# Kernel tuning notes

Hardware: AMD Instinct MI355X
Metric: run time of the kernel (lower is better)

## Reference

```python
import jax, jax.numpy as jnp
import numpy as np

NUM_HEADS = 4

def _pos_encoding(seq_len, d, dtype):
    # standard sinusoidal positional encoding [seq_len, d]
    pos = jnp.arange(seq_len, dtype=jnp.float32)[:, None]
    i = jnp.arange(0, d, 2, dtype=jnp.float32)
    div = jnp.exp(-jnp.log(10000.0) * i / d)
    ang = pos * div
    pe = jnp.zeros((seq_len, d), jnp.float32)
    pe = pe.at[:, 0::2].set(jnp.sin(ang)).at[:, 1::2].set(jnp.cos(ang))
    return pe.astype(dtype)

def _layer_norm(x, g, b, eps=1e-5):
    m = jnp.mean(x, axis=-1, keepdims=True)
    v = jnp.mean(jnp.square(x - m), axis=-1, keepdims=True)
    return (x - m) / jnp.sqrt(v + eps) * g + b

def setup_inputs() -> dict:
    key = jax.random.key(0)
    ks = jax.random.split(key, 10)
    B, S, H, W, N = 8, 512, 768, 8, 4096
    s = 0.02
    token_reps = jax.random.normal(ks[0], (B, S, H), jnp.float32)
    starts = jax.random.randint(ks[1], (B, N), 0, S - W)
    widths = jax.random.randint(ks[2], (B, N), 1, W + 1)
    span_ids = jnp.stack([starts, starts + widths], axis=-1)  # end > start, end <= S
    span_masks = jax.random.randint(ks[3], (B, N), 0, 2)
    return dict(
        token_reps=token_reps,
        dummy_query=jax.random.normal(ks[4], (H,), jnp.float32) * s,
        in_proj_w=jax.random.normal(ks[5], (3 * H, H), jnp.float32) * s,
        in_proj_b=jnp.zeros((3 * H,), jnp.float32),
        out_w=jax.random.normal(ks[6], (H, H), jnp.float32) * s,
        out_b=jnp.zeros((H,), jnp.float32),
        ln_g=jnp.ones((H,), jnp.float32),
        ln_b=jnp.zeros((H,), jnp.float32),
        ffn_w1=jax.random.normal(ks[7], (H, 4 * H), jnp.float32) * s,
        ffn_b1=jnp.zeros((4 * H,), jnp.float32),
        ffn_w2=jax.random.normal(ks[8], (4 * H, H), jnp.float32) * s,
        ffn_b2=jnp.zeros((H,), jnp.float32),
        span_ids=span_ids,
        span_masks=span_masks,
    )

def reference(token_reps, dummy_query, in_proj_w, in_proj_b, out_w, out_b,
              ln_g, ln_b, ffn_w1, ffn_b1, ffn_w2, ffn_b2, span_ids, span_masks):
    B, S, H = token_reps.shape
    N = span_ids.shape[1]
    NH = NUM_HEADS
    DH = H // NH
    # sequence positional encoding (dropout is identity in eval mode)
    x = token_reps + _pos_encoding(S, H, token_reps.dtype)[None]
    Wq, Wk, Wv = jnp.split(in_proj_w, 3, axis=0)
    bq, bk, bv = jnp.split(in_proj_b, 3)
    # single shared dummy query -> per-head query [NH, DH]
    q = (dummy_query @ Wq.T + bq).reshape(NH, DH)
    k = (x @ Wk.T + bk).reshape(B, S, NH, DH)
    v = (x @ Wv.T + bv).reshape(B, S, NH, DH)
    # scores are identical across spans since the query is shared: [B, NH, S]
    scores = jnp.einsum('hd,bshd->bhs', q, k) / jnp.sqrt(jnp.asarray(DH, x.dtype))
    pos = jnp.arange(S)
    # per-span key validity: start <= pos < end, and span not masked out  [B, N, S]
    valid = (pos[None, None, :] >= span_ids[..., 0:1]) & \
            (pos[None, None, :] < span_ids[..., 1:2]) & \
            (span_masks[..., None] != 0)
    logits = jnp.where(valid[:, :, None, :], scores[:, None, :, :], -1e9)  # [B,N,NH,S]
    w = jax.nn.softmax(logits, axis=-1)
    attn = jnp.einsum('bnhs,bshd->bnhd', w, v).reshape(B, N, H)
    attn = attn @ out_w.T + out_b
    h1 = _layer_norm(attn + dummy_query, ln_g, ln_b)
    ffn = jax.nn.relu(h1 @ ffn_w1 + ffn_b1) @ ffn_w2 + ffn_b2
    out = _layer_norm(ffn + h1, ln_g, ln_b)
    # masked spans produce exact zeros, matching the original loop
    return out * (span_masks[..., None] != 0).astype(out.dtype)
```

## Files before the change

kernel.cpp:

```cpp
#include <hip/hip_runtime.h>
#include <hip/hip_bf16.h>

#define Bb 8
#define Ss 512
#define Hh 768
#define NHh 4
#define Nn 4096
#define ROWS (Bb * Nn)
#define SCB 128

typedef _Float16 f16x8 __attribute__((ext_vector_type(8)));
typedef _Float16 f16x4 __attribute__((ext_vector_type(4)));
typedef _Float16 f16x2 __attribute__((ext_vector_type(2)));
typedef float f32x4 __attribute__((ext_vector_type(4)));

#define DEVINL __device__ __forceinline__

DEVINL void gld_lds16(const void* g, void* l) {
  __builtin_amdgcn_global_load_lds(
      (const __attribute__((address_space(1))) void*)g,
      (__attribute__((address_space(3))) void*)l, 16, 0, 0);
}

template <int V>
DEVINL void wait_vmcnt() {
  if constexpr (V == 0) asm volatile("s_waitcnt vmcnt(0)" ::: "memory");
  else if constexpr (V == 3) asm volatile("s_waitcnt vmcnt(3)" ::: "memory");
  else if constexpr (V == 4) asm volatile("s_waitcnt vmcnt(4)" ::: "memory");
  else if constexpr (V == 6) asm volatile("s_waitcnt vmcnt(6)" ::: "memory");
  else if constexpr (V == 8) asm volatile("s_waitcnt vmcnt(8)" ::: "memory");
}

DEVINL float block_sum256(float v, float* red) {
#pragma unroll
  for (int o = 32; o; o >>= 1) v += __shfl_xor(v, o, 64);
  const int wid = threadIdx.x >> 6, lane = threadIdx.x & 63;
  if (lane == 0) red[wid] = v;
  __syncthreads();
  float r = red[0] + red[1] + red[2] + red[3];
  __syncthreads();
  return r;
}

__global__ __launch_bounds__(256) void x_kernel(const float* __restrict__ tok,
                                                _Float16* __restrict__ x) {
  int idx = blockIdx.x * 256 + threadIdx.x;
  int t = idx % 384;
  int bs = idx / 384;
  int s = bs & (Ss - 1);
  float div = expf(-(float)t * 0.02398526138535465f);
  float ang = (float)s * div;
  float sv = sinf(ang), cv = cosf(ang);
  const float2 tv = ((const float2*)tok)[(size_t)bs * 384 + t];
  f16x2 o;
  o[0] = (_Float16)(tv.x + sv);
  o[1] = (_Float16)(tv.y + cv);
  *(f16x2*)&x[(size_t)bs * Hh + 2 * t] = o;
}

__global__ __launch_bounds__(256) void q_kernel(const float* __restrict__ dq,
                                                const float* __restrict__ ipw,
                                                const float* __restrict__ ipb,
                                                float* __restrict__ qout) {
  __shared__ float red[4];
  int o = blockIdx.x;
  const float* wr = ipw + (size_t)o * Hh;
  float s = 0.f;
#pragma unroll
  for (int e = 0; e < 3; e++) {
    int j = threadIdx.x + 256 * e;
    s += dq[j] * wr[j];
  }
  s = block_sum256(s, red);
  if (threadIdx.x == 0) qout[o] = s + ipb[o];
}

__global__ __launch_bounds__(256) void c_kernel(const float* __restrict__ q,
                                                const float* __restrict__ ipw,
                                                const float* __restrict__ ipb,
                                                float* __restrict__ cout,
                                                float* __restrict__ sbias) {
  __shared__ float red[4];
  int bid = blockIdx.x;
  int t = threadIdx.x;
  if (bid < 3072) {
    int h = bid / Hh;
    int j = bid - h * Hh;
    float s = 0.f;
    if (t < 192) s = q[h * 192 + t] * ipw[(size_t)(Hh + h * 192 + t) * Hh + j];
    s = block_sum256(s, red);
    if (t == 0) cout[bid] = s;
  } else {
    int h = bid - 3072;
    float s = 0.f;
    if (t < 192) s = q[h * 192 + t] * ipb[Hh + h * 192 + t];
    s = block_sum256(s, red);
    if (t == 0) sbias[h] = s;
  }
}

__global__ __launch_bounds__(256) void score_kernel(
    const _Float16* __restrict__ x, const float* __restrict__ c,
    const float* __restrict__ sbias, float* __restrict__ scores) {
  int bs = blockIdx.x;
  int wid = threadIdx.x >> 6, lane = threadIdx.x & 63;
  const _Float16* xr = x + (size_t)bs * Hh;
  const float* ch = c + wid * Hh;
  float s = 0.f;
#pragma unroll
  for (int e = 0; e < 12; e++) {
    int j = e * 64 + lane;
    s += (float)xr[j] * ch[j];
  }
#pragma unroll
  for (int o = 32; o; o >>= 1) s += __shfl_xor(s, o, 64);
  if (lane == 0) {
    int b = bs >> 9, pos = bs & (Ss - 1);
    scores[((size_t)(b * NHh + wid)) * Ss + pos] =
        (s + sbias[wid]) * 0.07216878364870322f;
  }
}

__global__ __launch_bounds__(256) void cvt_kernel(const float* __restrict__ in,
                                                  _Float16* __restrict__ out) {
  int i = blockIdx.x * 256 + threadIdx.x;
  float4 f = ((const float4*)in)[i];
  f16x4 o;
  o[0] = (_Float16)f.x;
  o[1] = (_Float16)f.y;
  o[2] = (_Float16)f.z;
  o[3] = (_Float16)f.w;
  ((f16x4*)out)[i] = o;
}

__global__ __launch_bounds__(256) void trcvt_kernel(const float* __restrict__ in,
                                                    _Float16* __restrict__ out,
                                                    int R, int C) {
  __shared__ float tile[32][33];
  int c0 = blockIdx.x * 32, r0 = blockIdx.y * 32;
  int tx = threadIdx.x & 31, ty0 = threadIdx.x >> 5;
#pragma unroll
  for (int ty = ty0; ty < 32; ty += 8)
    tile[ty][tx] = in[(size_t)(r0 + ty) * C + c0 + tx];
  __syncthreads();
#pragma unroll
  for (int ty = ty0; ty < 32; ty += 8)
    out[(size_t)(c0 + ty) * R + r0 + tx] = (_Float16)tile[tx][ty];
}

__global__ __launch_bounds__(256) void scan1_kernel(const int* __restrict__ mask,
                                                    int* __restrict__ bsum) {
  int r = blockIdx.x * 256 + threadIdx.x;
  unsigned long long b = __ballot(mask[r] != 0);
  __shared__ int wsum[4];
  int lane = threadIdx.x & 63, wid = threadIdx.x >> 6;
  if (lane == 0) wsum[wid] = __popcll(b);
  __syncthreads();
  if (threadIdx.x == 0)
    bsum[blockIdx.x] = wsum[0] + wsum[1] + wsum[2] + wsum[3];
}
__global__ __launch_bounds__(64) void scan2_kernel(const int* __restrict__ bsum,
                                                   int* __restrict__ boff,
                                                   int* __restrict__ cnt) {
  if (threadIdx.x == 0) {
    int acc = 0;
    for (int i = 0; i < SCB; i++) {
      boff[i] = acc;
      acc += bsum[i];
    }
    *cnt = acc;
  }
}
__global__ __launch_bounds__(256) void cidx_kernel(const int* __restrict__ mask,
                                                   const int* __restrict__ boff,
                                                   int* __restrict__ cidx) {
  int r = blockIdx.x * 256 + threadIdx.x;
  int m = mask[r] != 0;
  unsigned long long b = __ballot(m);
  __shared__ int wsum[4];
  int lane = threadIdx.x & 63, wid = threadIdx.x >> 6;
  if (lane == 0) wsum[wid] = __popcll(b);
  __syncthreads();
  int pre = 0;
#pragma unroll
  for (int i = 0; i < 3; i++)
    if (i < wid) pre += wsum[i];
  pre += __popcll(b & ((1ULL << lane) - 1));
  if (m) cidx[r] = boff[blockIdx.x] + pre;
}

template <int RELU, int BN>
__global__ __launch_bounds__(256, 2) void gemm_nt(
    const _Float16* __restrict__ A, const _Float16* __restrict__ W,
    const float* __restrict__ bias, _Float16* __restrict__ C, int N, int K,
    int nn, const int* __restrict__ mcount) {
  const int bid = (int)blockIdx.x;
  const int mi = (bid >> 3) / nn;
  const int nt_ = (bid >> 3) - mi * nn;
  const long m0 = (long)(mi * 8 + (bid & 7)) * 128;
  const long n0 = (long)nt_ * BN;
  if (mcount && m0 >= (long)*mcount) return;
  __shared__ __align__(16) _Float16 As[3][128 * 32];
  __shared__ __align__(16) _Float16 Bs[3][BN * 32];
  const int tid = threadIdx.x;
  const int wid = tid >> 6;
  const int lane = tid & 63;
  constexpr int LPS = (BN == 128) ? 4 : 3;

  const int c0 = wid * 64 + lane;
  const int c1 = c0 + 256;
  const int sw0 = ((c0 & 3) ^ ((c0 >> 3) & 3)) * 8;
  const int sw1 = ((c1 & 3) ^ ((c1 >> 3) & 3)) * 8;
  const _Float16* gA0 = A + (m0 + (c0 >> 2)) * K + sw0;
  const _Float16* gA1 = A + (m0 + (c1 >> 2)) * K + sw1;
  const _Float16* gB0 = W + (n0 + (c0 >> 2)) * K + sw0;
  const _Float16* gB1 = W + (n0 + (c1 >> 2)) * K + sw1;

  const int wr = (wid >> 1) * 64;
  const int wc = (wid & 1) * (BN / 2);
  constexpr int NF = BN / 32;
  const int fr = lane & 15;
  const int fkb = lane >> 4;

  f32x4 acc[4][NF];
#pragma unroll
  for (int mi2 = 0; mi2 < 4; mi2++)
#pragma unroll
    for (int ni = 0; ni < NF; ni++) acc[mi2][ni] = (f32x4){0.f, 0.f, 0.f, 0.f};

#define STAGE(buf, k0)                                                  \
  do {                                                                  \
    gld_lds16(gA0 + (k0), &As[buf][wid * 512]);                         \
    gld_lds16(gA1 + (k0), &As[buf][2048 + wid * 512]);                  \
    gld_lds16(gB0 + (k0), &Bs[buf][wid * 512]);                         \
    if constexpr (BN == 128) gld_lds16(gB1 + (k0), &Bs[buf][2048 + wid * 512]); \
  } while (0)

#define COMPUTE(buf)                                                          \
  do {                                                                        \
    f16x8 af[4], bf[NF];                                                      \
    _Pragma("unroll") for (int i = 0; i < 4; i++) {                           \
      int r_ = wr + i * 16 + fr;                                              \
      af[i] = *(const f16x8*)&As[buf][r_ * 32 + ((fkb ^ ((r_ >> 1) & 3)) * 8)]; \
    }                                                                         \
    _Pragma("unroll") for (int i = 0; i < NF; i++) {                          \
      int r_ = wc + i * 16 + fr;                                              \
      bf[i] = *(const f16x8*)&Bs[buf][r_ * 32 + ((fkb ^ ((r_ >> 1) & 3)) * 8)]; \
    }                                                                         \
    __builtin_amdgcn_s_setprio(1);                                            \
    _Pragma("unroll") for (int mi2 = 0; mi2 < 4; mi2++)                       \
        _Pragma("unroll") for (int ni = 0; ni < NF; ni++)                     \
            acc[mi2][ni] = __builtin_amdgcn_mfma_f32_16x16x32_f16(            \
                af[mi2], bf[ni], acc[mi2][ni], 0, 0, 0);                      \
    __builtin_amdgcn_s_setprio(0);                                            \
  } while (0)

#define ITER_RESTAGE(b, knext)              \
  do {                                      \
    wait_vmcnt<2 * LPS>();                  \
    __builtin_amdgcn_s_barrier();           \
    COMPUTE(b);                             \
    __builtin_amdgcn_s_barrier();           \
    STAGE(b, (knext));                      \
  } while (0)

  const int nt = K >> 5;
  STAGE(0, 0);
  STAGE(1, 32);
  STAGE(2, 64);
  int t = 0;
  for (; t <= nt - 6; t += 3) {
    ITER_RESTAGE(0, (t + 3) * 32);
    ITER_RESTAGE(1, (t + 4) * 32);
    ITER_RESTAGE(2, (t + 5) * 32);
  }
  wait_vmcnt<2 * LPS>();
  __builtin_amdgcn_s_barrier();
  COMPUTE(0);
  wait_vmcnt<LPS>();
  __builtin_amdgcn_s_barrier();
  COMPUTE(1);
  wait_vmcnt<0>();
  __builtin_amdgcn_s_barrier();
  COMPUTE(2);
#undef STAGE
#undef COMPUTE
#undef ITER_RESTAGE

  const int crow = (lane >> 4) * 4;
  const int ccol = lane & 15;
  float bv[NF];
#pragma unroll
  for (int ni = 0; ni < NF; ni++)
    bv[ni] = bias ? bias[n0 + wc + ni * 16 + ccol] : 0.f;
#pragma unroll
  for (int mi2 = 0; mi2 < 4; mi2++)
#pragma unroll
    for (int ni = 0; ni < NF; ni++)
#pragma unroll
      for (int i = 0; i < 4; i++) {
        float v = acc[mi2][ni][i] + bv[ni];
        if (RELU) v = fmaxf(v, 0.f);
        C[(m0 + wr + mi2 * 16 + crow + i) * (long)N + (n0 + wc + ni * 16 + ccol)] =
            (_Float16)v;
      }
}

template <int RELU>
__global__ __launch_bounds__(512, 4) void gemm8_nt(
    const _Float16* __restrict__ A, const _Float16* __restrict__ W,
    const float* __restrict__ bias, _Float16* __restrict__ C, int N, int K,
    int nn, const int* __restrict__ mcount) {
  const int bid = (int)blockIdx.x;
  const int mi = (bid >> 3) / nn;
  const int nt_ = (bid >> 3) - mi * nn;
  const long m0 = (long)(mi * 8 + (bid & 7)) * 256;
  const long n0 = (long)nt_ * 128;
  if (mcount && m0 >= (long)*mcount) return;
  __shared__ __align__(16) _Float16 As[3][256 * 32];
  __shared__ __align__(16) _Float16 Bs[3][128 * 32];
  const int tid = threadIdx.x;
  const int w = tid >> 6;
  const int lane = tid & 63;
  constexpr int LPS = 3;

  const int rA0 = w * 16 + (lane >> 2);
  const int rA1 = rA0 + 128;
  const int cb = lane & 3;
  const int swA0 = (cb ^ ((rA0 >> 1) & 3)) * 8;
  const int swA1 = (cb ^ ((rA1 >> 1) & 3)) * 8;
  const _Float16* gA0 = A + (m0 + rA0) * K + swA0;
  const _Float16* gA1 = A + (m0 + rA1) * K + swA1;
  const _Float16* gB0 = W + (n0 + rA0) * K + swA0;

  const int wr = (w >> 1) * 64;
  const int wc = (w & 1) * 64;
  const int fr = lane & 15;
  const int fkb = lane >> 4;

  f32x4 acc[4][4];
#pragma unroll
  for (int mi2 = 0; mi2 < 4; mi2++)
#pragma unroll
    for (int ni = 0; ni < 4; ni++) acc[mi2][ni] = (f32x4){0.f, 0.f, 0.f, 0.f};

#define STAGE(buf, k0)                                   \
  do {                                                   \
    gld_lds16(gA0 + (k0), &As[buf][w * 512]);            \
    gld_lds16(gA1 + (k0), &As[buf][(w + 8) * 512]);      \
    gld_lds16(gB0 + (k0), &Bs[buf][w * 512]);            \
  } while (0)

#define COMPUTE(buf)                                                          \
  do {                                                                        \
    f16x8 af[4], bf[4];                                                       \
    _Pragma("unroll") for (int i = 0; i < 4; i++) {                           \
      int r_ = wr + i * 16 + fr;                                              \
      af[i] = *(const f16x8*)&As[buf][r_ * 32 + ((fkb ^ ((r_ >> 1) & 3)) * 8)]; \
    }                                                                         \
    _Pragma("unroll") for (int i = 0; i < 4; i++) {                           \
      int r_ = wc + i * 16 + fr;                                              \
      bf[i] = *(const f16x8*)&Bs[buf][r_ * 32 + ((fkb ^ ((r_ >> 1) & 3)) * 8)]; \
    }                                                                         \
    __builtin_amdgcn_s_setprio(1);                                            \
    _Pragma("unroll") for (int mi2 = 0; mi2 < 4; mi2++)                       \
        _Pragma("unroll") for (int ni = 0; ni < 4; ni++)                      \
            acc[mi2][ni] = __builtin_amdgcn_mfma_f32_16x16x32_f16(            \
                af[mi2], bf[ni], acc[mi2][ni], 0, 0, 0);                      \
    __builtin_amdgcn_s_setprio(0);                                            \
  } while (0)

#define ITER_RESTAGE(b, knext)              \
  do {                                      \
    wait_vmcnt<2 * LPS>();                  \
    __builtin_amdgcn_s_barrier();           \
    COMPUTE(b);                             \
    __builtin_amdgcn_s_barrier();           \
    STAGE(b, (knext));                      \
  } while (0)

  const int nt = K >> 5;
  STAGE(0, 0);
  STAGE(1, 32);
  STAGE(2, 64);
  int t = 0;
  for (; t <= nt - 6; t += 3) {
    ITER_RESTAGE(0, (t + 3) * 32);
    ITER_RESTAGE(1, (t + 4) * 32);
    ITER_RESTAGE(2, (t + 5) * 32);
  }
  wait_vmcnt<2 * LPS>();
  __builtin_amdgcn_s_barrier();
  COMPUTE(0);
  wait_vmcnt<LPS>();
  __builtin_amdgcn_s_barrier();
  COMPUTE(1);
  wait_vmcnt<0>();
  __builtin_amdgcn_s_barrier();
  COMPUTE(2);
#undef STAGE
#undef COMPUTE
#undef ITER_RESTAGE

  const int crow = (lane >> 4) * 4;
  const int ccol = lane & 15;
  float bv[4];
#pragma unroll
  for (int ni = 0; ni < 4; ni++)
    bv[ni] = bias ? bias[n0 + wc + ni * 16 + ccol] : 0.f;
#pragma unroll
  for (int mi2 = 0; mi2 < 4; mi2++)
#pragma unroll
    for (int ni = 0; ni < 4; ni++)
#pragma unroll
      for (int i = 0; i < 4; i++) {
        float v = acc[mi2][ni][i] + bv[ni];
        if (RELU) v = fmaxf(v, 0.f);
        C[(m0 + wr + mi2 * 16 + crow + i) * (long)N + (n0 + wc + ni * 16 + ccol)] =
            (_Float16)v;
      }
}

template <int RELU>
__global__ __launch_bounds__(512, 2) void gemm16_nt(
    const _Float16* __restrict__ A, const _Float16* __restrict__ W,
    const float* __restrict__ bias, _Float16* __restrict__ C, int N, int K,
    int nn, const int* __restrict__ mcount) {
  const int bid = (int)blockIdx.x;
  const int mi = (bid >> 3) / nn;
  const int nt_ = (bid >> 3) - mi * nn;
  const long m0 = (long)(mi * 8 + (bid & 7)) * 256;
  const long n0 = (long)nt_ * 256;
  if (mcount && m0 >= (long)*mcount) return;
  __shared__ __align__(16) _Float16 As[3][256 * 32];
  __shared__ __align__(16) _Float16 Bs[3][256 * 32];
  const int tid = threadIdx.x;
  const int w = tid >> 6;
  const int lane = tid & 63;
  constexpr int LPS = 4;

  const int r0c = w * 16 + (lane >> 2);
  const int r1c = r0c + 128;
  const int cb = lane & 3;
  const int sw0 = (cb ^ ((r0c >> 1) & 3)) * 8;
  const int sw1 = (cb ^ ((r1c >> 1) & 3)) * 8;
  const _Float16* gA0 = A + (m0 + r0c) * K + sw0;
  const _Float16* gA1 = A + (m0 + r1c) * K + sw1;
  const _Float16* gB0 = W + (n0 + r0c) * K + sw0;
  const _Float16* gB1 = W + (n0 + r1c) * K + sw1;

  const int wr = (w >> 2) * 128;
  const int wc = (w & 3) * 64;
  const int fr = lane & 15;
  const int fkb = lane >> 4;

  f32x4 acc[8][4];
#pragma unroll
  for (int mi2 = 0; mi2 < 8; mi2++)
#pragma unroll
    for (int ni = 0; ni < 4; ni++) acc[mi2][ni] = (f32x4){0.f, 0.f, 0.f, 0.f};

#define STAGE(buf, k0)                                   \
  do {                                                   \
    gld_lds16(gA0 + (k0), &As[buf][w * 512]);            \
    gld_lds16(gA1 + (k0), &As[buf][(w + 8) * 512]);      \
    gld_lds16(gB0 + (k0), &Bs[buf][w * 512]);            \
    gld_lds16(gB1 + (k0), &Bs[buf][(w + 8) * 512]);      \
  } while (0)

#define COMPUTE(buf)                                                          \
  do {                                                                        \
    f16x8 af[8], bf[4];                                                       \
    _Pragma("unroll") for (int i = 0; i < 8; i++) {                           \
      int r_ = wr + i * 16 + fr;                                              \
      af[i] = *(const f16x8*)&As[buf][r_ * 32 + ((fkb ^ ((r_ >> 1) & 3)) * 8)]; \
    }                                                                         \
    _Pragma("unroll") for (int i = 0; i < 4; i++) {                           \
      int r_ = wc + i * 16 + fr;                                              \
      bf[i] = *(const f16x8*)&Bs[buf][r_ * 32 + ((fkb ^ ((r_ >> 1) & 3)) * 8)]; \
    }                                                                         \
    __builtin_amdgcn_s_setprio(1);                                            \
    _Pragma("unroll") for (int mi2 = 0; mi2 < 8; mi2++)                       \
        _Pragma("unroll") for (int ni = 0; ni < 4; ni++)                      \
            acc[mi2][ni] = __builtin_amdgcn_mfma_f32_16x16x32_f16(            \
                af[mi2], bf[ni], acc[mi2][ni], 0, 0, 0);                      \
    __builtin_amdgcn_s_setprio(0);                                            \
  } while (0)

#define ITER_RESTAGE(b, knext)              \
  do {                                      \
    wait_vmcnt<2 * LPS>();                  \
    __builtin_amdgcn_s_barrier();           \
    COMPUTE(b);                             \
    __builtin_amdgcn_s_barrier();           \
    STAGE(b, (knext));                      \
  } while (0)

  const int nt = K >> 5;
  STAGE(0, 0);
  STAGE(1, 32);
  STAGE(2, 64);
  int t = 0;
  for (; t <= nt - 6; t += 3) {
    ITER_RESTAGE(0, (t + 3) * 32);
    ITER_RESTAGE(1, (t + 4) * 32);
    ITER_RESTAGE(2, (t + 5) * 32);
  }
  wait_vmcnt<2 * LPS>();
  __builtin_amdgcn_s_barrier();
  COMPUTE(0);
  wait_vmcnt<LPS>();
  __builtin_amdgcn_s_barrier();
  COMPUTE(1);
  wait_vmcnt<0>();
  __builtin_amdgcn_s_barrier();
  COMPUTE(2);
#undef STAGE
#undef COMPUTE
#undef ITER_RESTAGE

  const int crow = (lane >> 4) * 4;
  const int ccol = lane & 15;
  float bv[4];
#pragma unroll
  for (int ni = 0; ni < 4; ni++)
    bv[ni] = bias ? bias[n0 + wc + ni * 16 + ccol] : 0.f;
#pragma unroll
  for (int mi2 = 0; mi2 < 8; mi2++)
#pragma unroll
    for (int ni = 0; ni < 4; ni++)
#pragma unroll
      for (int i = 0; i < 4; i++) {
        float v = acc[mi2][ni][i] + bv[ni];
        if (RELU) v = fmaxf(v, 0.f);
        C[(m0 + wr + mi2 * 16 + crow + i) * (long)N + (n0 + wc + ni * 16 + ccol)] =
            (_Float16)v;
      }
}

__global__ __launch_bounds__(192) void pool_kernel(
    const _Float16* __restrict__ v, const float* __restrict__ scores,
    const int* __restrict__ span_ids, const int* __restrict__ span_masks,
    _Float16* __restrict__ attn, const int* __restrict__ cidx) {
  int r = blockIdx.x;
  if (span_masks[r] == 0) return;
  int slot = cidx[r];
  int i = threadIdx.x;
  int h = i / 48;
  int d0 = i * 4;
  int b = r >> 12;
  int st = span_ids[2 * r], en = span_ids[2 * r + 1];
  int wdt = en - st;
  const float* sc = scores + ((size_t)(b * NHh + h)) * Ss + st;
  float w[8];
  float mx = -1e30f;
#pragma unroll
  for (int j = 0; j < 8; j++) {
    float t = (j < wdt) ? sc[j] : -1e30f;
    w[j] = t;
    mx = fmaxf(mx, t);
  }
  float sum = 0.f;
#pragma unroll
  for (int j = 0; j < 8; j++) {
    float e = (j < wdt) ? expf(w[j] - mx) : 0.f;
    w[j] = e;
    sum += e;
  }
  float inv = 1.f / sum;
  float a0 = 0.f, a1 = 0.f, a2 = 0.f, a3 = 0.f;
#pragma unroll
  for (int j = 0; j < 8; j++) {
    if (j < wdt) {
      f16x4 vv = *(const f16x4*)(v + ((size_t)(b * Ss + st + j)) * Hh + d0);
      float wj = w[j] * inv;
      a0 += wj * (float)vv[0];
      a1 += wj * (float)vv[1];
      a2 += wj * (float)vv[2];
      a3 += wj * (float)vv[3];
    }
  }
  f16x4 o;
  o[0] = (_Float16)a0;
  o[1] = (_Float16)a1;
  o[2] = (_Float16)a2;
  o[3] = (_Float16)a3;
  *(f16x4*)&attn[(size_t)slot * Hh + d0] = o;
}

__global__ __launch_bounds__(256) void ln0_kernel(
    _Float16* __restrict__ X, const float* __restrict__ AddV,
    const float* __restrict__ g, const float* __restrict__ bta,
    const int* __restrict__ mcount) {
  __shared__ float red[4];
  int r = blockIdx.x;
  if (r >= *mcount) return;
  int t = threadIdx.x;
  float xv[3];
#pragma unroll
  for (int e = 0; e < 3; e++) {
    int d = t + 256 * e;
    xv[e] = (float)X[(size_t)r * Hh + d] + AddV[d];
  }
  float s = xv[0] + xv[1] + xv[2];
  s = block_sum256(s, red);
  float mean = s * (1.f / 768.f);
  float vs = 0.f;
#pragma unroll
  for (int e = 0; e < 3; e++) {
    float d = xv[e] - mean;
    vs += d * d;
  }
  vs = block_sum256(vs, red);
  float inv = rsqrtf(vs * (1.f / 768.f) + 1e-5f);
#pragma unroll
  for (int e = 0; e < 3; e++) {
    int d = t + 256 * e;
    X[(size_t)r * Hh + d] = (_Float16)((xv[e] - mean) * inv * g[d] + bta[d]);
  }
}

__global__ __launch_bounds__(256) void ln1_kernel(
    const _Float16* __restrict__ F2c, const _Float16* __restrict__ h1c,
    const int* __restrict__ cidx, const float* __restrict__ g,
    const float* __restrict__ bta, const int* __restrict__ mask,
    float* __restrict__ out) {
  __shared__ float red[4];
  int r = blockIdx.x;
  int t = threadIdx.x;
  float* orow = out + (size_t)r * Hh;
  if (mask[r] == 0) {
#pragma unroll
    for (int e = 0; e < 3; e++) orow[t + 256 * e] = 0.f;
    return;
  }
  int c = cidx[r];
  float xv[3];
#pragma unroll
  for (int e = 0; e < 3; e++) {
    int d = t + 256 * e;
    xv[e] = (float)F2c[(size_t)c * Hh + d] + (float)h1c[(size_t)c * Hh + d];
  }
  float s = xv[0] + xv[1] + xv[2];
  s = block_sum256(s, red);
  float mean = s * (1.f / 768.f);
  float vs = 0.f;
#pragma unroll
  for (int e = 0; e < 3; e++) {
    float d = xv[e] - mean;
    vs += d * d;
  }
  vs = block_sum256(vs, red);
  float inv = rsqrtf(vs * (1.f / 768.f) + 1e-5f);
#pragma unroll
  for (int e = 0; e < 3; e++) {
    int d = t + 256 * e;
    orow[d] = (xv[e] - mean) * inv * g[d] + bta[d];
  }
}

extern "C" void kernel_launch(void* const* d_in, const int* in_sizes, int n_in,
                              void* d_out, int out_size, void* d_ws,
                              size_t ws_size, hipStream_t stream) {
  (void)out_size;
  if (n_in != 14) return;
  if (in_sizes[0] != 3145728 || in_sizes[2] != 1769472 ||
      in_sizes[3] != 2304 || in_sizes[4] != 589824 ||
      in_sizes[8] != 2359296 || in_sizes[9] != 3072 ||
      in_sizes[12] != 65536 || in_sizes[13] != 32768)
    return;

  const float* tok   = (const float*)d_in[0];
  const float* dq    = (const float*)d_in[1];
  const float* ipw   = (const float*)d_in[2];
  const float* ipb   = (const float*)d_in[3];
  const float* outw  = (const float*)d_in[4];
  const float* outb  = (const float*)d_in[5];
  const float* lng   = (const float*)d_in[6];
  const float* lnb   = (const float*)d_in[7];
  const float* w1    = (const float*)d_in[8];
  const float* b1    = (const float*)d_in[9];
  const float* w2    = (const float*)d_in[10];
  const float* b2    = (const float*)d_in[11];
  const int* spid    = (const int*)d_in[12];
  const int* spmask  = (const int*)d_in[13];

  char* ws = (char*)d_ws;
  size_t off = 0;
  auto alloc = [&](size_t bytes) {
    size_t r = off;
    off = (off + bytes + 255) & ~(size_t)255;
    return r;
  };
  _Float16* X16  = (_Float16*)(ws + alloc((size_t)Bb * Ss * Hh * 2));
  float* SC      = (float*)(ws + alloc((size_t)Bb * NHh * Ss * 4));
  float* Q       = (float*)(ws + alloc(768 * 4));
  float* Cc      = (float*)(ws + alloc(3072 * 4));
  float* SB      = (float*)(ws + alloc(4 * 4));
  _Float16* WV16 = (_Float16*)(ws + alloc((size_t)768 * 768 * 2));
  _Float16* OW16 = (_Float16*)(ws + alloc((size_t)768 * 768 * 2));
  _Float16* WT1  = (_Float16*)(ws + alloc((size_t)3072 * 768 * 2));
  _Float16* WT2  = (_Float16*)(ws + alloc((size_t)768 * 3072 * 2));
  _Float16* ATTN = (_Float16*)(ws + alloc((size_t)ROWS * Hh * 2));
  _Float16* PROJ = (_Float16*)(ws + alloc((size_t)ROWS * Hh * 2));
  _Float16* F1   = (_Float16*)(ws + alloc((size_t)ROWS * 3072 * 2));
  if (ws_size < off) return;
  _Float16* F2 = ATTN;

  int* CIDX = (int*)X16;
  int* BSUM = (int*)X16 + ROWS;
  int* BOFF = (int*)X16 + ROWS + SCB;
  int* CNT  = (int*)X16 + ROWS + 2 * SCB;

  _Float16* V16 = (_Float16*)d_out;

  cvt_kernel<<<576, 256, 0, stream>>>(ipw + (size_t)1536 * 768, WV16);
  cvt_kernel<<<576, 256, 0, stream>>>(outw, OW16);
  trcvt_kernel<<<dim3(96, 24), 256, 0, stream>>>(w1, WT1, 768, 3072);
  trcvt_kernel<<<dim3(24, 96), 256, 0, stream>>>(w2, WT2, 3072, 768);

  x_kernel<<<(Bb * Ss * 384) / 256, 256, 0, stream>>>(tok, X16);
  q_kernel<<<768, 256, 0, stream>>>(dq, ipw, ipb, Q);
  c_kernel<<<3076, 256, 0, stream>>>(Q, ipw, ipb, Cc, SB);
  score_kernel<<<Bb * Ss, 256, 0, stream>>>(X16, Cc, SB, SC);
  gemm_nt<0, 64><<<384, 256, 0, stream>>>(X16, WV16, ipb + 1536, V16,
                                          768, 768, 12, nullptr);
  scan1_kernel<<<SCB, 256, 0, stream>>>(spmask, BSUM);
  scan2_kernel<<<1, 64, 0, stream>>>(BSUM, BOFF, CNT);
  cidx_kernel<<<SCB, 256, 0, stream>>>(spmask, BOFF, CIDX);
  pool_kernel<<<ROWS, 192, 0, stream>>>(V16, SC, spid, spmask, ATTN, CIDX);
  gemm8_nt<0><<<768, 512, 0, stream>>>(ATTN, OW16, outb, PROJ,
                                       768, 768, 6, CNT);
  ln0_kernel<<<ROWS, 256, 0, stream>>>(PROJ, dq, lng, lnb, CNT);
  gemm16_nt<1><<<1536, 512, 0, stream>>>(PROJ, WT1, b1, F1,
                                         3072, 768, 12, CNT);
  gemm8_nt<0><<<768, 512, 0, stream>>>(F1, WT2, b2, F2,
                                       768, 3072, 6, CNT);
  ln1_kernel<<<ROWS, 256, 0, stream>>>(F2, PROJ, CIDX, lng, lnb, spmask,
                                       (float*)d_out);
}
```

Baseline: 379.6 us.

## Replace 16-wave FFN1 GEMM with 4-wave 256x128 tile kernel

The FFN up-projection GEMM moves from a 512-thread, 256x256-tile kernel to a 256-thread kernel with 256x128 tiles. Each of the 4 waves computes a 128x64 sub-tile and issues 6 global-to-LDS loads per stage. The grid doubles to 3072 blocks, and the shared pipeline body is pulled into a common macro. This trades B-tile reuse for smaller blocks, less LDS per block and possibly better occupancy, at the cost of more redundant A-tile loads.

```diff
diff --git a/kernel.cpp b/kernel.cpp
--- a/kernel.cpp
+++ b/kernel.cpp
@@ -29,6 +29,7 @@
   else if constexpr (V == 4) asm volatile("s_waitcnt vmcnt(4)" ::: "memory");
   else if constexpr (V == 6) asm volatile("s_waitcnt vmcnt(6)" ::: "memory");
   else if constexpr (V == 8) asm volatile("s_waitcnt vmcnt(8)" ::: "memory");
+  else if constexpr (V == 12) asm volatile("s_waitcnt vmcnt(12)" ::: "memory");
 }
 
 DEVINL float block_sum256(float v, float* red) {
@@ -189,6 +190,35 @@
   if (m) cidx[r] = boff[blockIdx.x] + pre;
 }
 
+#define ITER_RESTAGE(b, knext)              \
+  do {                                      \
+    wait_vmcnt<2 * LPS>();                  \
+    __builtin_amdgcn_s_barrier();           \
+    COMPUTE(b);                             \
+    __builtin_amdgcn_s_barrier();           \
+    STAGE(b, (knext));                      \
+  } while (0)
+#define PIPE_MAIN()                         \
+  const int nt = K >> 5;                    \
+  STAGE(0, 0);                              \
+  STAGE(1, 32);                             \
+  STAGE(2, 64);                             \
+  int t = 0;                                \
+  for (; t <= nt - 6; t += 3) {             \
+    ITER_RESTAGE(0, (t + 3) * 32);          \
+    ITER_RESTAGE(1, (t + 4) * 32);          \
+    ITER_RESTAGE(2, (t + 5) * 32);          \
+  }                                         \
+  wait_vmcnt<2 * LPS>();                    \
+  __builtin_amdgcn_s_barrier();             \
+  COMPUTE(0);                               \
+  wait_vmcnt<LPS>();                        \
+  __builtin_amdgcn_s_barrier();             \
+  COMPUTE(1);                               \
+  wait_vmcnt<0>();                          \
+  __builtin_amdgcn_s_barrier();             \
+  COMPUTE(2);
+
 template <int RELU, int BN>
 __global__ __launch_bounds__(256, 2) void gemm_nt(
     const _Float16* __restrict__ A, const _Float16* __restrict__ W,
@@ -255,37 +285,9 @@
     __builtin_amdgcn_s_setprio(0);                                            \
   } while (0)
 
-#define ITER_RESTAGE(b, knext)              \
-  do {                                      \
-    wait_vmcnt<2 * LPS>();                  \
-    __builtin_amdgcn_s_barrier();           \
-    COMPUTE(b);                             \
-    __builtin_amdgcn_s_barrier();           \
-    STAGE(b, (knext));                      \
-  } while (0)
-
-  const int nt = K >> 5;
-  STAGE(0, 0);
-  STAGE(1, 32);
-  STAGE(2, 64);
-  int t = 0;
-  for (; t <= nt - 6; t += 3) {
-    ITER_RESTAGE(0, (t + 3) * 32);
-    ITER_RESTAGE(1, (t + 4) * 32);
-    ITER_RESTAGE(2, (t + 5) * 32);
-  }
-  wait_vmcnt<2 * LPS>();
-  __builtin_amdgcn_s_barrier();
-  COMPUTE(0);
-  wait_vmcnt<LPS>();
-  __builtin_amdgcn_s_barrier();
-  COMPUTE(1);
-  wait_vmcnt<0>();
-  __builtin_amdgcn_s_barrier();
-  COMPUTE(2);
+  PIPE_MAIN()
 #undef STAGE
 #undef COMPUTE
-#undef ITER_RESTAGE
 
   const int crow = (lane >> 4) * 4;
   const int ccol = lane & 15;
@@ -370,37 +372,9 @@
     __builtin_amdgcn_s_setprio(0);                                            \
   } while (0)
 
-#define ITER_RESTAGE(b, knext)              \
-  do {                                      \
-    wait_vmcnt<2 * LPS>();                  \
-    __builtin_amdgcn_s_barrier();           \
-    COMPUTE(b);                             \
-    __builtin_amdgcn_s_barrier();           \
-    STAGE(b, (knext));                      \
-  } while (0)
-
-  const int nt = K >> 5;
-  STAGE(0, 0);
-  STAGE(1, 32);
-  STAGE(2, 64);
-  int t = 0;
-  for (; t <= nt - 6; t += 3) {
-    ITER_RESTAGE(0, (t + 3) * 32);
-    ITER_RESTAGE(1, (t + 4) * 32);
-    ITER_RESTAGE(2, (t + 5) * 32);
-  }
-  wait_vmcnt<2 * LPS>();
-  __builtin_amdgcn_s_barrier();
-  COMPUTE(0);
-  wait_vmcnt<LPS>();
-  __builtin_amdgcn_s_barrier();
-  COMPUTE(1);
-  wait_vmcnt<0>();
-  __builtin_amdgcn_s_barrier();
-  COMPUTE(2);
+  PIPE_MAIN()
 #undef STAGE
 #undef COMPUTE
-#undef ITER_RESTAGE
 
   const int crow = (lane >> 4) * 4;
   const int ccol = lane & 15;
@@ -422,7 +396,7 @@
 }
 
 template <int RELU>
-__global__ __launch_bounds__(512, 2) void gemm16_nt(
+__global__ __launch_bounds__(256, 2) void gemm4w_nt(
     const _Float16* __restrict__ A, const _Float16* __restrict__ W,
     const float* __restrict__ bias, _Float16* __restrict__ C, int N, int K,
     int nn, const int* __restrict__ mcount) {
@@ -430,27 +404,23 @@
   const int mi = (bid >> 3) / nn;
   const int nt_ = (bid >> 3) - mi * nn;
   const long m0 = (long)(mi * 8 + (bid & 7)) * 256;
-  const long n0 = (long)nt_ * 256;
+  const long n0 = (long)nt_ * 128;
   if (mcount && m0 >= (long)*mcount) return;
   __shared__ __align__(16) _Float16 As[3][256 * 32];
-  __shared__ __align__(16) _Float16 Bs[3][256 * 32];
+  __shared__ __align__(16) _Float16 Bs[3][128 * 32];
   const int tid = threadIdx.x;
   const int w = tid >> 6;
   const int lane = tid & 63;
-  constexpr int LPS = 4;
-
-  const int r0c = w * 16 + (lane >> 2);
-  const int r1c = r0c + 128;
+  constexpr int LPS = 6;
+
+  const int rA = w * 16 + (lane >> 2);
   const int cb = lane & 3;
-  const int sw0 = (cb ^ ((r0c >> 1) & 3)) * 8;
-  const int sw1 = (cb ^ ((r1c >> 1) & 3)) * 8;
-  const _Float16* gA0 = A + (m0 + r0c) * K + sw0;
-  const _Float16* gA1 = A + (m0 + r1c) * K + sw1;
-  const _Float16* gB0 = W + (n0 + r0c) * K + sw0;
-  const _Float16* gB1 = W + (n0 + r1c) * K + sw1;
-
-  const int wr = (w >> 2) * 128;
-  const int wc = (w & 3) * 64;
+  const int sw = (cb ^ ((rA >> 1) & 3)) * 8;
+  const _Float16* gA = A + (m0 + rA) * K + sw;
+  const _Float16* gB = W + (n0 + rA) * K + sw;
+
+  const int wr = (w >> 1) * 128;
+  const int wc = (w & 1) * 64;
   const int fr = lane & 15;
   const int fkb = lane >> 4;
 
@@ -460,12 +430,14 @@
 #pragma unroll
     for (int ni = 0; ni < 4; ni++) acc[mi2][ni] = (f32x4){0.f, 0.f, 0.f, 0.f};
 
-#define STAGE(buf, k0)                                   \
-  do {                                                   \
-    gld_lds16(gA0 + (k0), &As[buf][w * 512]);            \
-    gld_lds16(gA1 + (k0), &As[buf][(w + 8) * 512]);      \
-    gld_lds16(gB0 + (k0), &Bs[buf][w * 512]);            \
-    gld_lds16(gB1 + (k0), &Bs[buf][(w + 8) * 512]);      \
+#define STAGE(buf, k0)                                             \
+  do {                                                             \
+    gld_lds16(gA + (k0), &As[buf][w * 512]);                       \
+    gld_lds16(gA + (size_t)64 * K + (k0), &As[buf][(w + 4) * 512]);  \
+    gld_lds16(gA + (size_t)128 * K + (k0), &As[buf][(w + 8) * 512]); \
+    gld_lds16(gA + (size_t)192 * K + (k0), &As[buf][(w + 12) * 512]);\
+    gld_lds16(gB + (k0), &Bs[buf][w * 512]);                       \
+    gld_lds16(gB + (size_t)64 * K + (k0), &Bs[buf][(w + 4) * 512]);  \
   } while (0)
 
 #define COMPUTE(buf)                                                          \
@@ -487,37 +459,9 @@
     __builtin_amdgcn_s_setprio(0);                                            \
   } while (0)
 
-#define ITER_RESTAGE(b, knext)              \
-  do {                                      \
-    wait_vmcnt<2 * LPS>();                  \
-    __builtin_amdgcn_s_barrier();           \
-    COMPUTE(b);                             \
-    __builtin_amdgcn_s_barrier();           \
-    STAGE(b, (knext));                      \
-  } while (0)
-
-  const int nt = K >> 5;
-  STAGE(0, 0);
-  STAGE(1, 32);
-  STAGE(2, 64);
-  int t = 0;
-  for (; t <= nt - 6; t += 3) {
-    ITER_RESTAGE(0, (t + 3) * 32);
-    ITER_RESTAGE(1, (t + 4) * 32);
-    ITER_RESTAGE(2, (t + 5) * 32);
-  }
-  wait_vmcnt<2 * LPS>();
-  __builtin_amdgcn_s_barrier();
-  COMPUTE(0);
-  wait_vmcnt<LPS>();
-  __builtin_amdgcn_s_barrier();
-  COMPUTE(1);
-  wait_vmcnt<0>();
-  __builtin_amdgcn_s_barrier();
-  COMPUTE(2);
+  PIPE_MAIN()
 #undef STAGE
 #undef COMPUTE
-#undef ITER_RESTAGE
 
   const int crow = (lane >> 4) * 4;
   const int ccol = lane & 15;
@@ -732,8 +676,8 @@
   gemm8_nt<0><<<768, 512, 0, stream>>>(ATTN, OW16, outb, PROJ,
                                        768, 768, 6, CNT);
   ln0_kernel<<<ROWS, 256, 0, stream>>>(PROJ, dq, lng, lnb, CNT);
-  gemm16_nt<1><<<1536, 512, 0, stream>>>(PROJ, WT1, b1, F1,
-                                         3072, 768, 12, CNT);
+  gemm4w_nt<1><<<3072, 256, 0, stream>>>(PROJ, WT1, b1, F1,
+                                         3072, 768, 24, CNT);
   gemm8_nt<0><<<768, 512, 0, stream>>>(F1, WT2, b2, F2,
                                        768, 3072, 6, CNT);
   ln1_kernel<<<ROWS, 256, 0, stream>>>(F2, PROJ, CIDX, lng, lnb, spmask,
```

New measurement: 368.5 us. -2.9%, faster.
